# Optimization experiments

Measured on AMD Instinct MI355X. Metric: run time of the kernel, lower is better.

## Reference

```python
import jax, jax.numpy as jnp
from jax import lax
import numpy as np

T, B, I, U = 512, 64, 512, 512
FORGET_BIAS = 1.0  # matches forget_bias=1.0; cell_clip=None -> no clipping; no peephole


def setup_inputs() -> dict:
    key = jax.random.key(0)
    kx, kw = jax.random.split(key)
    x = jax.random.normal(kx, (T, B, I), dtype=jnp.float32)
    cs0 = jnp.zeros((B, U), dtype=jnp.float32)
    h0 = jnp.zeros((B, U), dtype=jnp.float32)
    # kernel [input_size + num_units, 4*num_units], bias [4*num_units] (zeros init as in build())
    w = jax.random.normal(kw, (I + U, 4 * U), dtype=jnp.float32) * 0.05
    b = jnp.zeros((4 * U,), dtype=jnp.float32)
    return {"x": x, "cs0": cs0, "h0": h0, "w": w, "b": b}


def reference(x, cs0, h0, w, b):
    """Fused BlockLSTM forward. Returns (h_seq [T,B,U], final_cs, final_h),
    mirroring LSTMBlockWrapper.call -> (outputs, (cell_state, output))."""

    def step(carry, x_t):
        cs_prev, h_prev = carry
        z = jnp.concatenate([x_t, h_prev], axis=-1) @ w + b  # [B, 4U]
        # TF BlockLSTM gate order: i, ci (cell input), f, o
        zi, zci, zf, zo = jnp.split(z, 4, axis=-1)
        i = jax.nn.sigmoid(zi)
        f = jax.nn.sigmoid(zf + FORGET_BIAS)
        ci = jnp.tanh(zci)
        cs = ci * i + cs_prev * f  # no cell_clip (cell_clip=-1)
        h = jnp.tanh(cs) * jax.nn.sigmoid(zo)
        return (cs, h), h

    (final_cs, final_h), h_seq = lax.scan(step, (cs0, h0), x)
    return h_seq, final_cs, final_h
```

## Files before the change

### kernel.cpp

```cpp
#include <hip/hip_runtime.h>


#define T_STEPS 512
#define NB 64
#define NU 512
#define NI 512
#define KTOT 1024
#define ZCOLS 2048
#define HSEQ_ELEMS (T_STEPS * NB * NU)
#define POISON64 0x7FC07FC07FC07FC0ull

typedef float    floatx4   __attribute__((ext_vector_type(4)));
typedef __bf16   bf16x8    __attribute__((ext_vector_type(8)));
typedef unsigned short ushortx8 __attribute__((ext_vector_type(8)));
typedef unsigned long long ull_t;

static __device__ __forceinline__ unsigned short f2bf(float f) {
  unsigned int u = __builtin_bit_cast(unsigned int, f);
  u += 0x7fffu + ((u >> 16) & 1u);
  return (unsigned short)(u >> 16);
}
static __device__ __forceinline__ float bf2f(unsigned short h) {
  unsigned int u = ((unsigned int)h) << 16;
  return __builtin_bit_cast(float, u);
}
static __device__ __forceinline__ float sigmoidf_(float x) {
  return __builtin_amdgcn_rcpf(1.0f + __expf(-x));
}
static __device__ __forceinline__ float fast_tanhf(float x) {
  const float ax = fabsf(x);
  const float t = __expf(-2.0f * ax);
  const float r = (1.0f - t) * __builtin_amdgcn_rcpf(1.0f + t);
  return copysignf(r, x);
}
static __device__ __forceinline__ bf16x8 ldfrag(const unsigned short* p) {
  ushortx8 v = *reinterpret_cast<const ushortx8*>(p);
  return __builtin_bit_cast(bf16x8, v);
}
static __device__ __forceinline__ ull_t pack4bf(float a, float b, float c, float d) {
  return (ull_t)f2bf(a) | ((ull_t)f2bf(b) << 16) | ((ull_t)f2bf(c) << 32) |
         ((ull_t)f2bf(d) << 48);
}
static __device__ __forceinline__ bf16x8 mkfrag(ull_t lo, ull_t hi) {
  struct P { ull_t a, b; } s{lo, hi};
  return __builtin_bit_cast(bf16x8, s);
}

__global__ __launch_bounds__(256) void init_kernel(const float* __restrict__ h0,
                                                   unsigned short* __restrict__ hbf) {
  const int j = blockIdx.x * 256 + threadIdx.x;
  if (j < 524288) {
    ull_t* p = reinterpret_cast<ull_t*>(&hbf[32768 + (size_t)j * 32]);
#pragma unroll
    for (int r = 0; r < 8; ++r) p[r] = POISON64;
  } else {
    const int k = j - 524288;
#pragma unroll
    for (int p2 = 0; p2 < 2; ++p2) {
      const int i = k * 2 + p2;
      const int row = i >> 6, chunk = i & 63;
      const float* src = &h0[row * NU + chunk * 8];
      const ull_t lo = pack4bf(src[0], src[4], src[1], src[5]);
      const ull_t hi = pack4bf(src[2], src[6], src[3], src[7]);
      const size_t off =
          (size_t)(chunk >> 2) * 2048 + (size_t)(chunk & 3) * 512 + (size_t)row * 8;
      *reinterpret_cast<ull_t*>(&hbf[off]) = lo;
      *reinterpret_cast<ull_t*>(&hbf[off + 4]) = hi;
    }
  }
}

__global__ __launch_bounds__(256) void transpose_w_kernel(
    const float* __restrict__ w, unsigned short* __restrict__ wT) {
  __shared__ float tile[32][33];
  const int u0 = blockIdx.x * 32;
  const int k0 = blockIdx.y * 32;
  const int g = blockIdx.z;
  const int tx = threadIdx.x & 31, ty = threadIdx.x >> 5;
#pragma unroll
  for (int r = 0; r < 4; ++r) {
    const int k = ty + r * 8;
    tile[k][tx] = w[(size_t)(k0 + k) * ZCOLS + g * 512 + u0 + tx];
  }
  __syncthreads();
#pragma unroll
  for (int r = 0; r < 4; ++r) {
    const int u = ty + r * 8;
    const int kk = k0 + tx;
    int kd = kk;
    if (kk >= 512) {
      const int u3 = kk & 7;
      kd = (kk & ~7) | (((u3 & 3) << 1) | (u3 >> 2));
    }
    wT[(size_t)((u0 + u) * 4 + g) * KTOT + kd] = f2bf(tile[tx][u]);
  }
}

__global__ __launch_bounds__(256) void gemm_zx_kernel(
    const float* __restrict__ x, const unsigned short* __restrict__ wT,
    const float* __restrict__ bias, unsigned short* __restrict__ zxp) {
  __shared__ __align__(16) unsigned short As[128][32];
  __shared__ __align__(16) unsigned short Bs[128][32];
  const int m0 = blockIdx.y * 128;
  const int n0 = blockIdx.x * 128;
  const int tid = threadIdx.x;
  const int wid = tid >> 6, lane = tid & 63;
  const int quad = lane >> 4, nl = lane & 15;
  const int wm = (wid & 1) * 64, wn = (wid >> 1) * 64;
  const int srow = tid >> 3;
  const int skk = (tid & 7) * 4;

  floatx4 acc[4][4] = {};

  for (int kt = 0; kt < 16; ++kt) {
    const int k0 = kt * 32;
    __syncthreads();
#pragma unroll
    for (int r = 0; r < 4; ++r) {
      const int row = r * 32 + srow;
      const float4 v =
          *reinterpret_cast<const float4*>(&x[(size_t)(m0 + row) * NI + k0 + skk]);
      *reinterpret_cast<ull_t*>(&As[row][skk]) = pack4bf(v.x, v.y, v.z, v.w);
      *reinterpret_cast<ull_t*>(&Bs[row][skk]) =
          *reinterpret_cast<const ull_t*>(&wT[(size_t)(n0 + row) * KTOT + k0 + skk]);
    }
    __syncthreads();
    bf16x8 af[4], bfr[4];
#pragma unroll
    for (int i = 0; i < 4; ++i) {
      af[i] = ldfrag(&As[wm + i * 16 + nl][quad * 8]);
      bfr[i] = ldfrag(&Bs[wn + i * 16 + nl][quad * 8]);
    }
#pragma unroll
    for (int i = 0; i < 4; ++i)
#pragma unroll
      for (int j = 0; j < 4; ++j)
        acc[i][j] =
            __builtin_amdgcn_mfma_f32_16x16x32_bf16(af[i], bfr[j], acc[i][j], 0, 0, 0);
  }

  float bv[4];
#pragma unroll
  for (int j = 0; j < 4; ++j) {
    const int colp = n0 + wn + j * 16 + nl;
    bv[j] = bias[(colp & 3) * 512 + (colp >> 2)];
  }
#pragma unroll
  for (int i = 0; i < 4; ++i) {
    const int browb = wm + i * 16 + quad * 4;
    const int t = (m0 + browb) >> 6;
    const int rt = (browb >> 5) & 1;
    const int hi = (browb & 31) >> 3;
    const int qb = (browb >> 2) & 1;
#pragma unroll
    for (int j = 0; j < 4; ++j) {
      const int colp = n0 + wn + j * 16 + nl;
      const int cbl = colp >> 5;
      const int lanep = (colp & 31) + 32 * qb;
      const ull_t packed =
          pack4bf(acc[i][j][0] + bv[j], acc[i][j][1] + bv[j],
                  acc[i][j][2] + bv[j], acc[i][j][3] + bv[j]);
      *reinterpret_cast<ull_t*>(
          &zxp[((((size_t)t * 64 + cbl) * 2 + rt) * 64 + lanep) * 16 + hi * 4]) = packed;
    }
  }
}

__global__ __launch_bounds__(64) void lstm_rec_kernel(
    const unsigned short* __restrict__ zxp, const unsigned short* __restrict__ wT,
    const float* __restrict__ cs_init, float* __restrict__ out,
    unsigned short* __restrict__ hbf) {
  const int lane = threadIdx.x;
  const int bid = blockIdx.x;
  const int cb = bid >> 2;
  const int qr = bid & 3;
  const int l15 = lane & 15, quad = lane >> 4;
  const int row = qr * 16 + l15;

  bf16x8 Wf[2][16];
#pragma unroll
  for (int cf = 0; cf < 2; ++cf)
#pragma unroll
    for (int kf = 0; kf < 16; ++kf)
      Wf[cf][kf] = ldfrag(
          &wT[(size_t)(cb * 32 + cf * 16 + l15) * KTOT + 512 + kf * 32 + quad * 8]);

  float csv[2];
  csv[0] = cs_init[row * NU + cb * 8 + quad];
  csv[1] = cs_init[row * NU + cb * 8 + 4 + quad];

  ull_t AL[16], AH[16];
  auto issueA = [&](int tt) {
    const unsigned short* p0 =
        hbf + (size_t)tt * 32768 + (size_t)quad * 512 + (size_t)row * 8;
#pragma unroll
    for (int kf = 0; kf < 16; ++kf) {
      const unsigned short* p = p0 + (size_t)kf * 2048;
      AL[kf] = __hip_atomic_load((const ull_t*)p, __ATOMIC_RELAXED,
                                 __HIP_MEMORY_SCOPE_AGENT);
      AH[kf] = __hip_atomic_load((const ull_t*)(p + 4), __ATOMIC_RELAXED,
                                 __HIP_MEMORY_SCOPE_AGENT);
    }
  };

  unsigned short zxv[8];
  const int rt_ = qr >> 1;
  const int qb_ = (l15 >> 2) & 1;
  const int hi_ = (qr & 1) * 2 + (l15 >> 3);
  const int rr_ = l15 & 3;
  auto issueZ = [&](int tt) {
    const size_t base = (((size_t)tt * 64 + cb) * 2 + rt_) * 64;
#pragma unroll
    for (int cf = 0; cf < 2; ++cf)
#pragma unroll
      for (int g = 0; g < 4; ++g) {
        const int c5 = cf * 16 + quad * 4 + g;
        zxv[cf * 4 + g] = zxp[(base + (size_t)(c5 + 32 * qb_)) * 16 + hi_ * 4 + rr_];
      }
  };

  issueA(0);
  issueZ(0);

  for (int t = 0; t < T_STEPS; ++t) {
    floatx4 z0, z1;
    int tries = 0;
    while (true) {
      floatx4 p00 = {0.f, 0.f, 0.f, 0.f}, p01 = {0.f, 0.f, 0.f, 0.f};
      floatx4 p10 = {0.f, 0.f, 0.f, 0.f}, p11 = {0.f, 0.f, 0.f, 0.f};
#pragma unroll
      for (int kf = 0; kf < 8; ++kf) {
        const bf16x8 hlo = mkfrag(AL[kf], AH[kf]);
        const bf16x8 hhi = mkfrag(AL[8 + kf], AH[8 + kf]);
        p00 = __builtin_amdgcn_mfma_f32_16x16x32_bf16(Wf[0][kf], hlo, p00, 0, 0, 0);
        p01 = __builtin_amdgcn_mfma_f32_16x16x32_bf16(Wf[1][kf], hlo, p01, 0, 0, 0);
        p10 = __builtin_amdgcn_mfma_f32_16x16x32_bf16(Wf[0][8 + kf], hhi, p10, 0, 0, 0);
        p11 = __builtin_amdgcn_mfma_f32_16x16x32_bf16(Wf[1][8 + kf], hhi, p11, 0, 0, 0);
      }
      z0 = p00 + p10;
      z1 = p01 + p11;
      const float s = ((z0[0] + z0[1]) + (z0[2] + z0[3])) +
                      ((z1[0] + z1[1]) + (z1[2] + z1[3]));
      if (!__any(s != s) || ++tries >= (1 << 16)) break;
      issueA(t);
    }

    float hout[2];
    {
      const float iv = sigmoidf_(z0[0] + bf2f(zxv[0]));
      const float civ = fast_tanhf(z0[1] + bf2f(zxv[1]));
      const float fv = sigmoidf_(z0[2] + bf2f(zxv[2]) + 1.0f);
      const float ov = sigmoidf_(z0[3] + bf2f(zxv[3]));
      csv[0] = civ * iv + csv[0] * fv;
      hout[0] = fast_tanhf(csv[0]) * ov;
    }
    {
      const float iv = sigmoidf_(z1[0] + bf2f(zxv[4]));
      const float civ = fast_tanhf(z1[1] + bf2f(zxv[5]));
      const float fv = sigmoidf_(z1[2] + bf2f(zxv[6]) + 1.0f);
      const float ov = sigmoidf_(z1[3] + bf2f(zxv[7]));
      csv[1] = civ * iv + csv[1] * fv;
      hout[1] = fast_tanhf(csv[1]) * ov;
    }

    unsigned short* hw = &hbf[(size_t)(t + 1) * 32768 + (size_t)(cb >> 2) * 2048 +
                              (size_t)(cb & 3) * 512 + (size_t)row * 8 + 2 * quad];
    const unsigned hv = (unsigned)f2bf(hout[0]) | ((unsigned)f2bf(hout[1]) << 16);
    __hip_atomic_store(reinterpret_cast<unsigned*>(hw), hv, __ATOMIC_RELAXED,
                       __HIP_MEMORY_SCOPE_AGENT);

    if (t + 1 < T_STEPS) {
      issueA(t + 1);
      issueZ(t + 1);
    }

    float* op = &out[((size_t)t * NB + row) * NU + cb * 8];
    op[quad] = hout[0];
    op[4 + quad] = hout[1];
    if (t == T_STEPS - 1) {
      float* cp = &out[HSEQ_ELEMS + (size_t)row * NU + cb * 8];
      cp[quad] = csv[0];
      cp[4 + quad] = csv[1];
      float* hp2 = &out[HSEQ_ELEMS + NB * NU + (size_t)row * NU + cb * 8];
      hp2[quad] = hout[0];
      hp2[4 + quad] = hout[1];
    }
  }
}

extern "C" void kernel_launch(void* const* d_in, const int* in_sizes, int n_in,
                              void* d_out, int out_size, void* d_ws, size_t ws_size,
                              hipStream_t stream) {
  const float* x = (const float*)d_in[0];
  const float* cs0 = (const float*)d_in[1];
  const float* h0 = (const float*)d_in[2];
  const float* w = (const float*)d_in[3];
  const float* bias = (const float*)d_in[4];
  float* out = (float*)d_out;

  char* ws = (char*)d_ws;
  unsigned short* wT = (unsigned short*)(ws);
  unsigned short* zxp = (unsigned short*)(ws + (size_t)(4 << 20));
  unsigned short* hbf = (unsigned short*)(ws + (size_t)(132 << 20));

  init_kernel<<<dim3(2056), 256, 0, stream>>>(h0, hbf);
  transpose_w_kernel<<<dim3(16, 32, 4), 256, 0, stream>>>(w, wT);
  gemm_zx_kernel<<<dim3(16, 256), 256, 0, stream>>>(x, wT, bias, zxp);
  lstm_rec_kernel<<<dim3(256), 64, 0, stream>>>(zxp, wT, cs0, out, hbf);
}
```

Before: 1.305 ms.

## Pack eight recurrent waves per block and stage h through shared LDS

The recurrent kernel moves from 256 single-wave blocks to 32 blocks of 512 threads. Each block now loads the previous step's h vector from global memory once, cooperatively, polls for NaN poison per staged chunk, and waits on a block barrier (syncthreads_count) before all waves read MFMA operands from double-buffered padded LDS. The block's own freshly computed h columns go straight into LDS, so those chunks skip the global round trip. This cuts redundant global polling and per-wave spin traffic. In exchange every step adds block-wide barriers, and only 32 CUs take part.

Result: slower. 1.999 ms (+53.1%).

```diff
diff --git a/kernel.cpp b/kernel.cpp
--- a/kernel.cpp
+++ b/kernel.cpp
@@ -9,6 +9,7 @@
 #define ZCOLS 2048
 #define HSEQ_ELEMS (T_STEPS * NB * NU)
 #define POISON64 0x7FC07FC07FC07FC0ull
+#define CHUNK_STRIDE 272
 
 typedef float    floatx4   __attribute__((ext_vector_type(4)));
 typedef __bf16   bf16x8    __attribute__((ext_vector_type(8)));
@@ -22,6 +23,9 @@
 }
 static __device__ __forceinline__ float bf2f(unsigned short h) {
   unsigned int u = ((unsigned int)h) << 16;
+  return __builtin_bit_cast(float, u);
+}
+static __device__ __forceinline__ float asf(unsigned int u) {
   return __builtin_bit_cast(float, u);
 }
 static __device__ __forceinline__ float sigmoidf_(float x) {
@@ -41,9 +45,9 @@
   return (ull_t)f2bf(a) | ((ull_t)f2bf(b) << 16) | ((ull_t)f2bf(c) << 32) |
          ((ull_t)f2bf(d) << 48);
 }
-static __device__ __forceinline__ bf16x8 mkfrag(ull_t lo, ull_t hi) {
-  struct P { ull_t a, b; } s{lo, hi};
-  return __builtin_bit_cast(bf16x8, s);
+static __device__ __forceinline__ ull_t ld_agent8(const unsigned short* p) {
+  return __hip_atomic_load((const ull_t*)p, __ATOMIC_RELAXED,
+                           __HIP_MEMORY_SCOPE_AGENT);
 }
 
 __global__ __launch_bounds__(256) void init_kernel(const float* __restrict__ h0,
@@ -166,16 +170,21 @@
   }
 }
 
-__global__ __launch_bounds__(64) void lstm_rec_kernel(
+__global__ __launch_bounds__(512) void lstm_rec_kernel(
     const unsigned short* __restrict__ zxp, const unsigned short* __restrict__ wT,
     const float* __restrict__ cs_init, float* __restrict__ out,
     unsigned short* __restrict__ hbf) {
-  const int lane = threadIdx.x;
+  const int tid = threadIdx.x;
+  const int w = tid >> 6, lane = tid & 63;
+  const int l15 = lane & 15, quad = lane >> 4;
   const int bid = blockIdx.x;
-  const int cb = bid >> 2;
-  const int qr = bid & 3;
-  const int l15 = lane & 15, quad = lane >> 4;
+  const int ub = bid >> 2, qr = bid & 3;
+  const int cb = ub * 8 + w;
   const int row = qr * 16 + l15;
+  const int c = tid >> 3, sub = tid & 7;
+  const bool own = (c >> 3) == ub;
+
+  __shared__ __align__(16) char lsh[2][64 * CHUNK_STRIDE];
 
   bf16x8 Wf[2][16];
 #pragma unroll
@@ -188,20 +197,6 @@
   float csv[2];
   csv[0] = cs_init[row * NU + cb * 8 + quad];
   csv[1] = cs_init[row * NU + cb * 8 + 4 + quad];
-
-  ull_t AL[16], AH[16];
-  auto issueA = [&](int tt) {
-    const unsigned short* p0 =
-        hbf + (size_t)tt * 32768 + (size_t)quad * 512 + (size_t)row * 8;
-#pragma unroll
-    for (int kf = 0; kf < 16; ++kf) {
-      const unsigned short* p = p0 + (size_t)kf * 2048;
-      AL[kf] = __hip_atomic_load((const ull_t*)p, __ATOMIC_RELAXED,
-                                 __HIP_MEMORY_SCOPE_AGENT);
-      AH[kf] = __hip_atomic_load((const ull_t*)(p + 4), __ATOMIC_RELAXED,
-                                 __HIP_MEMORY_SCOPE_AGENT);
-    }
-  };
 
   unsigned short zxv[8];
   const int rt_ = qr >> 1;
@@ -219,31 +214,64 @@
       }
   };
 
-  issueA(0);
+  ull_t S0, S1, S2, S3;
+  auto stageIssue = [&](int tt) {
+    const unsigned short* p =
+        hbf + (size_t)tt * 32768 + (size_t)c * 512 + qr * 128 + sub * 16;
+    S0 = ld_agent8(p);
+    S1 = ld_agent8(p + 4);
+    S2 = ld_agent8(p + 8);
+    S3 = ld_agent8(p + 12);
+  };
+  auto stageOk = [&]() -> bool {
+    const float s = (asf((unsigned)(S0 & 0xffffffffu)) + asf((unsigned)(S0 >> 32))) +
+                    (asf((unsigned)(S1 & 0xffffffffu)) + asf((unsigned)(S1 >> 32))) +
+                    (asf((unsigned)(S2 & 0xffffffffu)) + asf((unsigned)(S2 >> 32))) +
+                    (asf((unsigned)(S3 & 0xffffffffu)) + asf((unsigned)(S3 >> 32)));
+    return s == s;
+  };
+  auto stageWrite = [&](int buf) {
+    ull_t* d = reinterpret_cast<ull_t*>(&lsh[buf][c * CHUNK_STRIDE + sub * 32]);
+    d[0] = S0; d[1] = S1; d[2] = S2; d[3] = S3;
+  };
+
+  bool okp = false;
+  stageIssue(0);
   issueZ(0);
 
   for (int t = 0; t < T_STEPS; ++t) {
-    floatx4 z0, z1;
-    int tries = 0;
+    const int buf = t & 1;
+
+    int guard = 0;
     while (true) {
-      floatx4 p00 = {0.f, 0.f, 0.f, 0.f}, p01 = {0.f, 0.f, 0.f, 0.f};
-      floatx4 p10 = {0.f, 0.f, 0.f, 0.f}, p11 = {0.f, 0.f, 0.f, 0.f};
-#pragma unroll
-      for (int kf = 0; kf < 8; ++kf) {
-        const bf16x8 hlo = mkfrag(AL[kf], AH[kf]);
-        const bf16x8 hhi = mkfrag(AL[8 + kf], AH[8 + kf]);
-        p00 = __builtin_amdgcn_mfma_f32_16x16x32_bf16(Wf[0][kf], hlo, p00, 0, 0, 0);
-        p01 = __builtin_amdgcn_mfma_f32_16x16x32_bf16(Wf[1][kf], hlo, p01, 0, 0, 0);
-        p10 = __builtin_amdgcn_mfma_f32_16x16x32_bf16(Wf[0][8 + kf], hhi, p10, 0, 0, 0);
-        p11 = __builtin_amdgcn_mfma_f32_16x16x32_bf16(Wf[1][8 + kf], hhi, p11, 0, 0, 0);
+      if (!okp) {
+        if (stageOk()) {
+          stageWrite(buf);
+          okp = true;
+        } else {
+          stageIssue(t);
+        }
       }
-      z0 = p00 + p10;
-      z1 = p01 + p11;
-      const float s = ((z0[0] + z0[1]) + (z0[2] + z0[3])) +
-                      ((z1[0] + z1[1]) + (z1[2] + z1[3]));
-      if (!__any(s != s) || ++tries >= (1 << 16)) break;
-      issueA(t);
-    }
+      if (__syncthreads_count((int)okp) == 512) break;
+      if (++guard >= (1 << 16)) break;
+    }
+
+    const char* lb = lsh[buf];
+    floatx4 p00 = {0.f, 0.f, 0.f, 0.f}, p01 = {0.f, 0.f, 0.f, 0.f};
+    floatx4 p10 = {0.f, 0.f, 0.f, 0.f}, p11 = {0.f, 0.f, 0.f, 0.f};
+#pragma unroll
+    for (int kf = 0; kf < 8; ++kf) {
+      const bf16x8 hlo = ldfrag(reinterpret_cast<const unsigned short*>(
+          lb + (kf * 4 + quad) * CHUNK_STRIDE + l15 * 16));
+      const bf16x8 hhi = ldfrag(reinterpret_cast<const unsigned short*>(
+          lb + ((kf + 8) * 4 + quad) * CHUNK_STRIDE + l15 * 16));
+      p00 = __builtin_amdgcn_mfma_f32_16x16x32_bf16(Wf[0][kf], hlo, p00, 0, 0, 0);
+      p01 = __builtin_amdgcn_mfma_f32_16x16x32_bf16(Wf[1][kf], hlo, p01, 0, 0, 0);
+      p10 = __builtin_amdgcn_mfma_f32_16x16x32_bf16(Wf[0][8 + kf], hhi, p10, 0, 0, 0);
+      p11 = __builtin_amdgcn_mfma_f32_16x16x32_bf16(Wf[1][8 + kf], hhi, p11, 0, 0, 0);
+    }
+    const floatx4 z0 = p00 + p10;
+    const floatx4 z1 = p01 + p11;
 
     float hout[2];
     {
@@ -263,14 +291,17 @@
       hout[1] = fast_tanhf(csv[1]) * ov;
     }
 
+    const unsigned hv = (unsigned)f2bf(hout[0]) | ((unsigned)f2bf(hout[1]) << 16);
     unsigned short* hw = &hbf[(size_t)(t + 1) * 32768 + (size_t)(cb >> 2) * 2048 +
                               (size_t)(cb & 3) * 512 + (size_t)row * 8 + 2 * quad];
-    const unsigned hv = (unsigned)f2bf(hout[0]) | ((unsigned)f2bf(hout[1]) << 16);
     __hip_atomic_store(reinterpret_cast<unsigned*>(hw), hv, __ATOMIC_RELAXED,
                        __HIP_MEMORY_SCOPE_AGENT);
 
     if (t + 1 < T_STEPS) {
-      issueA(t + 1);
+      *reinterpret_cast<unsigned*>(
+          &lsh[buf ^ 1][cb * CHUNK_STRIDE + l15 * 16 + quad * 4]) = hv;
+      okp = own;
+      if (!own) stageIssue(t + 1);
       issueZ(t + 1);
     }
 
@@ -306,5 +337,5 @@
   init_kernel<<<dim3(2056), 256, 0, stream>>>(h0, hbf);
   transpose_w_kernel<<<dim3(16, 32, 4), 256, 0, stream>>>(w, wT);
   gemm_zx_kernel<<<dim3(16, 256), 256, 0, stream>>>(x, wT, bias, zxp);
-  lstm_rec_kernel<<<dim3(256), 64, 0, stream>>>(zxp, wT, cs0, out, hbf);
-}
+  lstm_rec_kernel<<<dim3(32), 512, 0, stream>>>(zxp, wT, cs0, out, hbf);
+}
```
